# Optimization experiments

Measured on AMD Instinct MI355X. Metric: run time of the kernel, lower is better.

The kernel has to match this reference:

```python
import jax, jax.numpy as jnp
import numpy as np

DIM = 1024
HEADS = 16
HEAD_DIM = DIM // HEADS
B, N = 8, 1024


def setup_inputs() -> dict:
    key = jax.random.key(0)
    ks = jax.random.split(key, 10)
    s = lambda fan_in: 1.0 / np.sqrt(fan_in)
    return {
        "x": jax.random.normal(ks[0], (B, N, DIM), jnp.float32),
        "pose_angles": jax.random.normal(ks[1], (B, 3), jnp.float32),
        # weights stored (in, out) so y = x @ W + b (equivalent to torch Linear)
        "Wqkv": jax.random.normal(ks[2], (DIM, 3 * DIM), jnp.float32) * s(DIM),
        "bqkv": jnp.zeros((3 * DIM,), jnp.float32),
        "W1": jax.random.normal(ks[3], (3, 64), jnp.float32) * s(3),
        "b1": jnp.zeros((64,), jnp.float32),
        "W2": jax.random.normal(ks[4], (64, 3 * DIM), jnp.float32) * s(64),
        "b2": jnp.zeros((3 * DIM,), jnp.float32),
        "Wproj": jax.random.normal(ks[5], (DIM, DIM), jnp.float32) * s(DIM),
        "bproj": jnp.zeros((DIM,), jnp.float32),
    }


def reference(x, pose_angles, Wqkv, bqkv, W1, b1, W2, b2, Wproj, bproj):
    Bq, Nq, C = x.shape
    H, D = HEADS, HEAD_DIM
    # qkv projection -> [B,N,3,H,D] -> [3,B,H,N,D]
    qkv = (x @ Wqkv + bqkv).reshape(Bq, Nq, 3, H, D).transpose(2, 0, 3, 1, 4)
    q, k, v = qkv[0], qkv[1], qkv[2]
    # pose MLP: 3 -> 64 -> 3*dim, chunked into per-head biases [B,H,1,D]
    pose_emb = jax.nn.relu(pose_angles @ W1 + b1) @ W2 + b2
    pose_q, pose_k, pose_v = jnp.split(pose_emb, 3, axis=1)
    pose_q = pose_q.reshape(Bq, H, 1, D)
    pose_k = pose_k.reshape(Bq, H, 1, D)
    pose_v = pose_v.reshape(Bq, H, 1, D)
    q = q + pose_q
    k = k + pose_k
    v = v + pose_v
    scale = 1.0 / jnp.sqrt(jnp.asarray(D, x.dtype))
    attn = jax.nn.softmax(jnp.einsum("bhnd,bhmd->bhnm", q, k) * scale, axis=-1)
    # dropout is identity in eval mode
    out = jnp.einsum("bhnm,bhmd->bhnd", attn, v)
    out = out.transpose(0, 2, 1, 3).reshape(Bq, Nq, C)
    return out @ Wproj + bproj
```

## Files before the change

### kernel.cpp

```cpp
#include <hip/hip_runtime.h>
#include <stdint.h>

typedef unsigned short u16;
typedef short bf16x8 __attribute__((ext_vector_type(8)));
typedef short bf16x4 __attribute__((ext_vector_type(4)));
typedef float f32x4 __attribute__((ext_vector_type(4)));
typedef u16 u16x4 __attribute__((ext_vector_type(4)));

__device__ __forceinline__ u16 f2bf(float f) {
  union { float f; unsigned int u; } v; v.f = f;
  unsigned int r = v.u + 0x7fffu + ((v.u >> 16) & 1u);
  return (u16)(r >> 16);
}

__device__ __forceinline__ void async16(const void* g, void* l) {
  __builtin_amdgcn_global_load_lds(
      (const __attribute__((address_space(1))) unsigned int*)g,
      (__attribute__((address_space(3))) unsigned int*)l, 16, 0, 0);
}

__device__ __forceinline__ f32x4 mfma16x16(bf16x4 a, bf16x4 b, f32x4 c) {
#if __has_builtin(__builtin_amdgcn_mfma_f32_16x16x16bf16_1k)
  return __builtin_amdgcn_mfma_f32_16x16x16bf16_1k(a, b, c, 0, 0, 0);
#else
  asm volatile("v_mfma_f32_16x16x16_bf16 %0, %1, %2, %0\n\ts_nop 7\n\ts_nop 7"
               : "+v"(c) : "v"(a), "v"(b));
  return c;
#endif
}

__global__ void __launch_bounds__(256) front_kernel(
    const float4* __restrict__ x4, u16x4* __restrict__ xh4,
    const float* __restrict__ ang, const float* __restrict__ W1,
    const float* __restrict__ b1, const float* __restrict__ W2,
    const float* __restrict__ b2, float* __restrict__ pose,
    const float* __restrict__ Wqkv, u16* __restrict__ wqkvt,
    const float* __restrict__ Wproj, u16* __restrict__ wprojt) {
  __shared__ float sh[64 * 65];
  const int fb = blockIdx.x, t = threadIdx.x;
  if (fb < 96) {
    float (*hid)[64] = (float (*)[64])sh;
    for (int idx = t; idx < 512; idx += 256) {
      int b = idx >> 6, j = idx & 63;
      float a = b1[j];
#pragma unroll
      for (int i = 0; i < 3; ++i) a += ang[b * 3 + i] * W1[i * 64 + j];
      hid[b][j] = fmaxf(a, 0.f);
    }
    __syncthreads();
    int idx = fb * 256 + t;
    int b = idx / 3072, c = idx - b * 3072;
    float a = b2[c];
#pragma unroll
    for (int j = 0; j < 64; ++j) a += hid[b][j] * W2[j * 3072 + c];
    pose[idx] = a;
  } else if (fb < 1120) {
    const int n4 = 8 * 1024 * 1024 / 4;
    int i = (fb - 96) * 256 + t;
    const int stride = 1024 * 256;
    for (; i < n4; i += stride) {
      float4 v = x4[i];
      u16x4 o;
      o[0] = f2bf(v.x); o[1] = f2bf(v.y); o[2] = f2bf(v.z); o[3] = f2bf(v.w);
      xh4[i] = o;
    }
  } else {
    const float* W; u16* Wt; int Kdim, Ncol, bx, by;
    if (fb < 1888) { W = Wqkv; Wt = wqkvt; Kdim = 1024; Ncol = 3072;
                     int b = fb - 1120; bx = b % 48; by = b / 48; }
    else           { W = Wproj; Wt = wprojt; Kdim = 1024; Ncol = 1024;
                     int b = fb - 1888; bx = b % 16; by = b / 16; }
    float (*tile)[65] = (float (*)[65])sh;
    const int tx = t & 63, ty = t >> 6;
    const int c0 = bx * 64, k0 = by * 64;
#pragma unroll
    for (int rr = 0; rr < 16; ++rr) {
      int row = rr * 4 + ty;
      tile[row][tx] = W[(size_t)(k0 + row) * Ncol + c0 + tx];
    }
    __syncthreads();
#pragma unroll
    for (int rr = 0; rr < 16; ++rr) {
      int row = rr * 4 + ty;
      Wt[(size_t)(c0 + row) * Kdim + k0 + tx] = f2bf(tile[tx][row]);
    }
  }
}

template <int EPI>
__global__ void __launch_bounds__(512) gemm8_kernel(
    const u16* __restrict__ A, const u16* __restrict__ Bt,
    const float* __restrict__ bias, const float* __restrict__ pose,
    u16* __restrict__ qout, u16* __restrict__ kout, u16* __restrict__ vtout,
    float* __restrict__ cout, int Kdim, int Ncols, int nTilesX) {
  constexpr int BOFF = 256 * 64;
  __shared__ u16 lds[2][(256 + 128) * 64];
  const int t = threadIdx.x, l = t & 63, w = t >> 6;
  const int g = l >> 4, r16 = l & 15;
  const int wr = w >> 1, wc = w & 1;
  const int xk = r16 & 7;
  const int blk = blockIdx.x;
  const int xcd = blk & 7, c = blk >> 3;
  const int m0 = (xcd * 4 + (c & 3)) * 256;
  const int n0 = (c >> 2) * 128;
  (void)nTilesX;
  const u16* Ab = A + (size_t)m0 * Kdim;
  const u16* Bb = Bt + (size_t)n0 * Kdim;

  auto stage = [&](int buf, int kt, int st) {
#pragma unroll
    for (int it = 0; it < 2; ++it) {
      int idx = it * 512 + t, row = idx >> 3;
      int seg = (idx & 7) ^ (row & 7);
      if (st < 2)
        async16(Ab + (size_t)(st * 128 + row) * Kdim + kt + seg * 8,
                &lds[buf][st * 128 * 64 + idx * 8]);
      else
        async16(Bb + (size_t)row * Kdim + kt + seg * 8, &lds[buf][BOFF + idx * 8]);
    }
  };

  f32x4 acc[4][4] = {};
  const int nT = Kdim >> 6;
#pragma unroll
  for (int st = 0; st < 3; ++st) stage(0, 0, st);

  for (int tt = 0; tt < nT; ++tt) {
    const int cur = tt & 1, nxt = cur ^ 1;
    const bool pf = (tt + 1 < nT);
    const int ktn = (tt + 1) << 6;
    if (pf) {
      stage(nxt, ktn, 0);
      __builtin_amdgcn_sched_barrier(0);
      asm volatile("s_waitcnt vmcnt(2)" ::: "memory");
    } else {
      asm volatile("s_waitcnt vmcnt(0)" ::: "memory");
    }
    __builtin_amdgcn_s_barrier();
    __builtin_amdgcn_sched_barrier(0);
    bf16x8 bfr[4][2], af[2][2];
#pragma unroll
    for (int nj = 0; nj < 4; ++nj)
#pragma unroll
      for (int ks = 0; ks < 2; ++ks)
        bfr[nj][ks] = *(const bf16x8*)&lds[cur][BOFF + (wc * 64 + nj * 16 + r16) * 64 +
                                               ((ks * 4 + g) ^ xk) * 8];
#pragma unroll
    for (int mi = 0; mi < 2; ++mi)
#pragma unroll
      for (int ks = 0; ks < 2; ++ks)
        af[mi][ks] = *(const bf16x8*)&lds[cur][(wr * 64 + mi * 16 + r16) * 64 +
                                              ((ks * 4 + g) ^ xk) * 8];
    __builtin_amdgcn_s_setprio(1);
#pragma unroll
    for (int ks = 0; ks < 2; ++ks)
#pragma unroll
      for (int mi = 0; mi < 2; ++mi)
#pragma unroll
        for (int nj = 0; nj < 4; ++nj)
          acc[mi][nj] = __builtin_amdgcn_mfma_f32_16x16x32_bf16(af[mi][ks], bfr[nj][ks],
                                                                acc[mi][nj], 0, 0, 0);
    __builtin_amdgcn_s_setprio(0);
    if (pf) { stage(nxt, ktn, 1); stage(nxt, ktn, 2); }
    bf16x8 af2[2][2];
#pragma unroll
    for (int mi = 0; mi < 2; ++mi)
#pragma unroll
      for (int ks = 0; ks < 2; ++ks)
        af2[mi][ks] = *(const bf16x8*)&lds[cur][(wr * 64 + (mi + 2) * 16 + r16) * 64 +
                                               ((ks * 4 + g) ^ xk) * 8];
    __builtin_amdgcn_s_setprio(1);
#pragma unroll
    for (int ks = 0; ks < 2; ++ks)
#pragma unroll
      for (int mi = 0; mi < 2; ++mi)
#pragma unroll
        for (int nj = 0; nj < 4; ++nj)
          acc[mi + 2][nj] = __builtin_amdgcn_mfma_f32_16x16x32_bf16(af2[mi][ks], bfr[nj][ks],
                                                                    acc[mi + 2][nj], 0, 0, 0);
    __builtin_amdgcn_s_setprio(0);
    __builtin_amdgcn_s_barrier();
  }

#pragma unroll
  for (int mi = 0; mi < 4; ++mi)
#pragma unroll
    for (int nj = 0; nj < 4; ++nj)
#pragma unroll
      for (int r = 0; r < 4; ++r) {
        int row = m0 + wr * 64 + mi * 16 + g * 4 + r;
        int col = n0 + wc * 64 + nj * 16 + r16;
        float v = acc[mi][nj][r] + bias[col];
        if (EPI == 0) {
          int b = row >> 10, n = row & 1023;
          v += pose[b * 3072 + col];
          u16 hv = f2bf(v);
          int three = col >> 10, hh = (col >> 6) & 15, d = col & 63;
          size_t bhh = (size_t)(b * 16 + hh);
          if (three == 0)      qout[(bhh * 1024 + n) * 64 + d] = hv;
          else if (three == 1) kout[(bhh * 1024 + n) * 64 + d] = hv;
          else                 vtout[(bhh * 64 + d) * 1024 + n] = hv;
        } else {
          cout[(size_t)row * Ncols + col] = v;
        }
      }
}

__global__ void __launch_bounds__(256) attn_kernel(
    const u16* __restrict__ Qb, const u16* __restrict__ Kb,
    const u16* __restrict__ Vtb, u16* __restrict__ aout) {
  __shared__ u16 ldsK[2][64][72];
  __shared__ u16 ldsV[2][64][72];
  const int t = threadIdx.x, l = t & 63, w = t >> 6;
  const int g = l >> 4, r16 = l & 15;
  const int blk = blockIdx.x;
  const int bh = blk & 127, qt = blk >> 7;
  const int b = bh >> 4, h = bh & 15;
  const int q0 = qt * 64 + w * 16;
  const u16* Qp = Qb + ((size_t)bh * 1024 + q0 + r16) * 64;
  bf16x8 qreg0 = *(const bf16x8*)(Qp + g * 8);
  bf16x8 qreg1 = *(const bf16x8*)(Qp + 32 + g * 8);
  const u16* Kbase = Kb + (size_t)bh * 1024 * 64;
  const u16* Vbase = Vtb + (size_t)bh * 64 * 1024;
  const float cexp = 0.18033688f;

  const int row0 = t >> 3, seg0 = t & 7;
  const int row1 = (256 + t) >> 3, seg1 = t & 7;
  bf16x8 kreg0, kreg1, vreg0, vreg1;
  auto gload = [&](int key0) {
    kreg0 = *(const bf16x8*)(Kbase + (size_t)(key0 + row0) * 64 + seg0 * 8);
    vreg0 = *(const bf16x8*)(Vbase + (size_t)row0 * 1024 + key0 + seg0 * 8);
    kreg1 = *(const bf16x8*)(Kbase + (size_t)(key0 + row1) * 64 + seg1 * 8);
    vreg1 = *(const bf16x8*)(Vbase + (size_t)row1 * 1024 + key0 + seg1 * 8);
  };
  auto lwrite = [&](int buf) {
    *(bf16x8*)&ldsK[buf][row0][seg0 * 8] = kreg0;
    *(bf16x8*)&ldsV[buf][row0][seg0 * 8] = vreg0;
    *(bf16x8*)&ldsK[buf][row1][seg1 * 8] = kreg1;
    *(bf16x8*)&ldsV[buf][row1][seg1 * 8] = vreg1;
  };

  float m = -3e38f, rs = 0.f;
  f32x4 o[4] = {};
  gload(0); lwrite(0);
  __syncthreads();
  int cur = 0;
  for (int kt = 0; kt < 16; ++kt) {
    const bool pf = (kt + 1 < 16);
    if (pf) gload((kt + 1) * 64);
    f32x4 s[4] = {};
#pragma unroll
    for (int f = 0; f < 4; ++f) {
      bf16x8 ak0 = *(const bf16x8*)&ldsK[cur][f * 16 + r16][g * 8];
      s[f] = __builtin_amdgcn_mfma_f32_16x16x32_bf16(ak0, qreg0, s[f], 0, 0, 0);
      bf16x8 ak1 = *(const bf16x8*)&ldsK[cur][f * 16 + r16][32 + g * 8];
      s[f] = __builtin_amdgcn_mfma_f32_16x16x32_bf16(ak1, qreg1, s[f], 0, 0, 0);
    }
    float m01, m23, mt = -3e38f;
#pragma unroll
    for (int f = 0; f < 4; ++f) {
      m01 = fmaxf(s[f][0], s[f][1]);
      m23 = fmaxf(s[f][2], s[f][3]);
      mt = fmaxf(mt, fmaxf(m01, m23));
    }
    mt = fmaxf(mt, __shfl_xor(mt, 16));
    mt = fmaxf(mt, __shfl_xor(mt, 32));
    if (!__all(mt - m <= 64.f)) {
      float mnew = fmaxf(m, mt);
      float alpha = exp2f((m - mnew) * cexp);
      float ar[4];
#pragma unroll
      for (int r = 0; r < 4; ++r) ar[r] = __shfl(alpha, (l & 48) | (g * 4 + r));
#pragma unroll
      for (int nf = 0; nf < 4; ++nf)
#pragma unroll
        for (int r = 0; r < 4; ++r) o[nf][r] *= ar[r];
      rs *= alpha;
      m = mnew;
    }
    float rt = 0.f;
    bf16x4 pa[4];
#pragma unroll
    for (int f = 0; f < 4; ++f) {
#pragma unroll
      for (int r = 0; r < 4; ++r) {
        float p = exp2f((s[f][r] - m) * cexp);
        rt += p;
        pa[f][r] = (short)f2bf(p);
      }
    }
    rt += __shfl_xor(rt, 16);
    rt += __shfl_xor(rt, 32);
    rs += rt;
#pragma unroll
    for (int s4 = 0; s4 < 4; ++s4)
#pragma unroll
      for (int nf = 0; nf < 4; ++nf) {
        bf16x4 bv = *(const bf16x4*)&ldsV[cur][nf * 16 + r16][s4 * 16 + g * 4];
        o[nf] = mfma16x16(pa[s4], bv, o[nf]);
      }
    if (pf) lwrite(cur ^ 1);
    __syncthreads();
    cur ^= 1;
  }
  float rr[4];
#pragma unroll
  for (int r = 0; r < 4; ++r) rr[r] = __shfl(1.0f / rs, (l & 48) | (g * 4 + r));
#pragma unroll
  for (int nf = 0; nf < 4; ++nf)
#pragma unroll
    for (int r = 0; r < 4; ++r) {
      int qq = qt * 64 + w * 16 + g * 4 + r;
      int d = nf * 16 + r16;
      aout[((size_t)b * 1024 + qq) * 1024 + h * 64 + d] = f2bf(o[nf][r] * rr[r]);
    }
}

extern "C" void kernel_launch(void* const* d_in, const int* in_sizes, int n_in,
                              void* d_out, int out_size, void* d_ws, size_t ws_size,
                              hipStream_t stream) {
  (void)in_sizes; (void)n_in; (void)out_size; (void)ws_size;
  const float* x     = (const float*)d_in[0];
  const float* ang   = (const float*)d_in[1];
  const float* Wqkv  = (const float*)d_in[2];
  const float* bqkv  = (const float*)d_in[3];
  const float* W1    = (const float*)d_in[4];
  const float* b1    = (const float*)d_in[5];
  const float* W2    = (const float*)d_in[6];
  const float* b2    = (const float*)d_in[7];
  const float* Wproj = (const float*)d_in[8];
  const float* bproj = (const float*)d_in[9];
  float* out = (float*)d_out;
  char* ws = (char*)d_ws;

  u16* xh     = (u16*)(ws);
  u16* wqkvt  = (u16*)(ws + (size_t)16 * 1024 * 1024);
  u16* wprojt = (u16*)(ws + (size_t)22 * 1024 * 1024);
  float* pose = (float*)(ws + (size_t)24 * 1024 * 1024);
  u16* Qb     = (u16*)(ws + (size_t)25 * 1024 * 1024);
  u16* Kb     = (u16*)(ws + (size_t)41 * 1024 * 1024);
  u16* Vtb    = (u16*)(ws + (size_t)57 * 1024 * 1024);

  front_kernel<<<2144, 256, 0, stream>>>((const float4*)x, (u16x4*)xh,
                                         ang, W1, b1, W2, b2, pose,
                                         Wqkv, wqkvt, Wproj, wprojt);
  gemm8_kernel<0><<<768, 512, 0, stream>>>(xh, wqkvt, bqkv, pose,
                                           Qb, Kb, Vtb, nullptr, 1024, 3072, 24);
  attn_kernel<<<2048, 256, 0, stream>>>(Qb, Kb, Vtb, xh);
  gemm8_kernel<1><<<256, 512, 0, stream>>>(xh, wprojt, bproj, nullptr,
                                           nullptr, nullptr, nullptr, out, 1024, 1024, 8);
}
```

Baseline: 198.3 us.

## Replace double-buffered 256x128 GEMM with single-buffered 128x128 tile kernel

Both GEMMs switch from a 512-thread kernel with a 256x128 tile, double-buffered async LDS staging and priority hints to a simpler 256-thread kernel with a 128x128 tile and a single LDS buffer. Each K step loads, then syncs, then computes. The smaller tile doubles the block count and cuts LDS use per block, which could raise occupancy and help the smaller projection GEMM fill the GPU. In exchange it drops the load/compute overlap and reuses each loaded tile less, so the kernel will rely on having several blocks resident per CU to hide memory latency.

Result: faster. 194.1 us, median of 2 (-2.1%).

```diff
diff --git a/kernel.cpp b/kernel.cpp
--- a/kernel.cpp
+++ b/kernel.cpp
@@ -88,109 +88,66 @@
 }
 
 template <int EPI>
-__global__ void __launch_bounds__(512) gemm8_kernel(
+__global__ void __launch_bounds__(256) gemm97_kernel(
     const u16* __restrict__ A, const u16* __restrict__ Bt,
     const float* __restrict__ bias, const float* __restrict__ pose,
     u16* __restrict__ qout, u16* __restrict__ kout, u16* __restrict__ vtout,
-    float* __restrict__ cout, int Kdim, int Ncols, int nTilesX) {
-  constexpr int BOFF = 256 * 64;
-  __shared__ u16 lds[2][(256 + 128) * 64];
+    float* __restrict__ cout, int Kdim, int Ncols) {
+  __shared__ u16 ldsA[128 * 64];
+  __shared__ u16 ldsB[128 * 64];
   const int t = threadIdx.x, l = t & 63, w = t >> 6;
   const int g = l >> 4, r16 = l & 15;
   const int wr = w >> 1, wc = w & 1;
   const int xk = r16 & 7;
   const int blk = blockIdx.x;
   const int xcd = blk & 7, c = blk >> 3;
-  const int m0 = (xcd * 4 + (c & 3)) * 256;
-  const int n0 = (c >> 2) * 128;
-  (void)nTilesX;
+  const int m0 = (xcd * 8 + (c & 7)) * 128;
+  const int n0 = (c >> 3) * 128;
   const u16* Ab = A + (size_t)m0 * Kdim;
   const u16* Bb = Bt + (size_t)n0 * Kdim;
 
-  auto stage = [&](int buf, int kt, int st) {
-#pragma unroll
-    for (int it = 0; it < 2; ++it) {
-      int idx = it * 512 + t, row = idx >> 3;
+  f32x4 acc[4][4] = {};
+  for (int kt = 0; kt < Kdim; kt += 64) {
+#pragma unroll
+    for (int ii = 0; ii < 4; ++ii) {
+      int idx = ii * 256 + t, row = idx >> 3;
       int seg = (idx & 7) ^ (row & 7);
-      if (st < 2)
-        async16(Ab + (size_t)(st * 128 + row) * Kdim + kt + seg * 8,
-                &lds[buf][st * 128 * 64 + idx * 8]);
-      else
-        async16(Bb + (size_t)row * Kdim + kt + seg * 8, &lds[buf][BOFF + idx * 8]);
-    }
-  };
-
-  f32x4 acc[4][4] = {};
-  const int nT = Kdim >> 6;
-#pragma unroll
-  for (int st = 0; st < 3; ++st) stage(0, 0, st);
-
-  for (int tt = 0; tt < nT; ++tt) {
-    const int cur = tt & 1, nxt = cur ^ 1;
-    const bool pf = (tt + 1 < nT);
-    const int ktn = (tt + 1) << 6;
-    if (pf) {
-      stage(nxt, ktn, 0);
-      __builtin_amdgcn_sched_barrier(0);
-      asm volatile("s_waitcnt vmcnt(2)" ::: "memory");
-    } else {
-      asm volatile("s_waitcnt vmcnt(0)" ::: "memory");
-    }
-    __builtin_amdgcn_s_barrier();
-    __builtin_amdgcn_sched_barrier(0);
-    bf16x8 bfr[4][2], af[2][2];
-#pragma unroll
-    for (int nj = 0; nj < 4; ++nj)
-#pragma unroll
-      for (int ks = 0; ks < 2; ++ks)
-        bfr[nj][ks] = *(const bf16x8*)&lds[cur][BOFF + (wc * 64 + nj * 16 + r16) * 64 +
-                                               ((ks * 4 + g) ^ xk) * 8];
-#pragma unroll
-    for (int mi = 0; mi < 2; ++mi)
-#pragma unroll
-      for (int ks = 0; ks < 2; ++ks)
-        af[mi][ks] = *(const bf16x8*)&lds[cur][(wr * 64 + mi * 16 + r16) * 64 +
-                                              ((ks * 4 + g) ^ xk) * 8];
-    __builtin_amdgcn_s_setprio(1);
-#pragma unroll
-    for (int ks = 0; ks < 2; ++ks)
-#pragma unroll
-      for (int mi = 0; mi < 2; ++mi)
-#pragma unroll
-        for (int nj = 0; nj < 4; ++nj)
-          acc[mi][nj] = __builtin_amdgcn_mfma_f32_16x16x32_bf16(af[mi][ks], bfr[nj][ks],
-                                                                acc[mi][nj], 0, 0, 0);
-    __builtin_amdgcn_s_setprio(0);
-    if (pf) { stage(nxt, ktn, 1); stage(nxt, ktn, 2); }
-    bf16x8 af2[2][2];
-#pragma unroll
-    for (int mi = 0; mi < 2; ++mi)
-#pragma unroll
-      for (int ks = 0; ks < 2; ++ks)
-        af2[mi][ks] = *(const bf16x8*)&lds[cur][(wr * 64 + (mi + 2) * 16 + r16) * 64 +
-                                               ((ks * 4 + g) ^ xk) * 8];
-    __builtin_amdgcn_s_setprio(1);
-#pragma unroll
-    for (int ks = 0; ks < 2; ++ks)
-#pragma unroll
-      for (int mi = 0; mi < 2; ++mi)
-#pragma unroll
-        for (int nj = 0; nj < 4; ++nj)
-          acc[mi + 2][nj] = __builtin_amdgcn_mfma_f32_16x16x32_bf16(af2[mi][ks], bfr[nj][ks],
-                                                                    acc[mi + 2][nj], 0, 0, 0);
-    __builtin_amdgcn_s_setprio(0);
-    __builtin_amdgcn_s_barrier();
+      async16(Ab + (size_t)row * Kdim + kt + seg * 8, &ldsA[idx * 8]);
+    }
+#pragma unroll
+    for (int ii = 0; ii < 4; ++ii) {
+      int idx = ii * 256 + t, row = idx >> 3;
+      int seg = (idx & 7) ^ (row & 7);
+      async16(Bb + (size_t)row * Kdim + kt + seg * 8, &ldsB[idx * 8]);
+    }
+    __syncthreads();
+#pragma unroll
+    for (int ks = 0; ks < 2; ++ks) {
+      bf16x8 a[4], bb[4];
+#pragma unroll
+      for (int i = 0; i < 4; ++i)
+        a[i] = *(const bf16x8*)&ldsA[(wr * 64 + i * 16 + r16) * 64 + ((ks * 4 + g) ^ xk) * 8];
+#pragma unroll
+      for (int j = 0; j < 4; ++j)
+        bb[j] = *(const bf16x8*)&ldsB[(wc * 64 + j * 16 + r16) * 64 + ((ks * 4 + g) ^ xk) * 8];
+#pragma unroll
+      for (int i = 0; i < 4; ++i)
+#pragma unroll
+        for (int j = 0; j < 4; ++j)
+          acc[i][j] = __builtin_amdgcn_mfma_f32_16x16x32_bf16(a[i], bb[j], acc[i][j], 0, 0, 0);
+    }
+    __syncthreads();
   }
 
 #pragma unroll
-  for (int mi = 0; mi < 4; ++mi)
-#pragma unroll
-    for (int nj = 0; nj < 4; ++nj)
+  for (int i = 0; i < 4; ++i)
+#pragma unroll
+    for (int j = 0; j < 4; ++j)
 #pragma unroll
       for (int r = 0; r < 4; ++r) {
-        int row = m0 + wr * 64 + mi * 16 + g * 4 + r;
-        int col = n0 + wc * 64 + nj * 16 + r16;
-        float v = acc[mi][nj][r] + bias[col];
+        int row = m0 + wr * 64 + i * 16 + g * 4 + r;
+        int col = n0 + wc * 64 + j * 16 + r16;
+        float v = acc[i][j][r] + bias[col];
         if (EPI == 0) {
           int b = row >> 10, n = row & 1023;
           v += pose[b * 3072 + col];
@@ -344,9 +301,9 @@
   front_kernel<<<2144, 256, 0, stream>>>((const float4*)x, (u16x4*)xh,
                                          ang, W1, b1, W2, b2, pose,
                                          Wqkv, wqkvt, Wproj, wprojt);
-  gemm8_kernel<0><<<768, 512, 0, stream>>>(xh, wqkvt, bqkv, pose,
-                                           Qb, Kb, Vtb, nullptr, 1024, 3072, 24);
+  gemm97_kernel<0><<<1536, 256, 0, stream>>>(xh, wqkvt, bqkv, pose,
+                                             Qb, Kb, Vtb, nullptr, 1024, 3072);
   attn_kernel<<<2048, 256, 0, stream>>>(Qb, Kb, Vtb, xh);
-  gemm8_kernel<1><<<256, 512, 0, stream>>>(xh, wprojt, bproj, nullptr,
-                                           nullptr, nullptr, nullptr, out, 1024, 1024, 8);
-}
+  gemm97_kernel<1><<<512, 256, 0, stream>>>(xh, wprojt, bproj, nullptr,
+                                            nullptr, nullptr, nullptr, out, 1024, 1024);
+}
```

## Replace double-buffered pipelined GEMM with single-buffered LDS staging

Applied to the files above, without the earlier changes.

The GEMM kernel drops its two-stage LDS double buffer and the staggered prefetch of the next K tile. Each iteration now loads the whole A and B tile, synchronizes, computes all MFMAs, then synchronizes again. This halves LDS use per block, which may let more blocks fit per CU so that other blocks hide the memory latency. The cost is that load/compute overlap inside a block is lost, and there is more barrier stalling.

New measurement: 215.6 us. +8.7%, slower.

```diff
diff --git a/kernel.cpp b/kernel.cpp
--- a/kernel.cpp
+++ b/kernel.cpp
@@ -88,13 +88,13 @@
 }
 
 template <int EPI>
-__global__ void __launch_bounds__(512) gemm8_kernel(
+__global__ void __launch_bounds__(512) gemm_sb_kernel(
     const u16* __restrict__ A, const u16* __restrict__ Bt,
     const float* __restrict__ bias, const float* __restrict__ pose,
     u16* __restrict__ qout, u16* __restrict__ kout, u16* __restrict__ vtout,
-    float* __restrict__ cout, int Kdim, int Ncols, int nTilesX) {
+    float* __restrict__ cout, int Kdim, int Ncols) {
   constexpr int BOFF = 256 * 64;
-  __shared__ u16 lds[2][(256 + 128) * 64];
+  __shared__ u16 lds[(256 + 128) * 64];
   const int t = threadIdx.x, l = t & 63, w = t >> 6;
   const int g = l >> 4, r16 = l & 15;
   const int wr = w >> 1, wc = w & 1;
@@ -103,83 +103,56 @@
   const int xcd = blk & 7, c = blk >> 3;
   const int m0 = (xcd * 4 + (c & 3)) * 256;
   const int n0 = (c >> 2) * 128;
-  (void)nTilesX;
   const u16* Ab = A + (size_t)m0 * Kdim;
   const u16* Bb = Bt + (size_t)n0 * Kdim;
 
-  auto stage = [&](int buf, int kt, int st) {
-#pragma unroll
-    for (int it = 0; it < 2; ++it) {
-      int idx = it * 512 + t, row = idx >> 3;
-      int seg = (idx & 7) ^ (row & 7);
-      if (st < 2)
-        async16(Ab + (size_t)(st * 128 + row) * Kdim + kt + seg * 8,
-                &lds[buf][st * 128 * 64 + idx * 8]);
-      else
-        async16(Bb + (size_t)row * Kdim + kt + seg * 8, &lds[buf][BOFF + idx * 8]);
-    }
-  };
-
   f32x4 acc[4][4] = {};
   const int nT = Kdim >> 6;
-#pragma unroll
-  for (int st = 0; st < 3; ++st) stage(0, 0, st);
-
   for (int tt = 0; tt < nT; ++tt) {
-    const int cur = tt & 1, nxt = cur ^ 1;
-    const bool pf = (tt + 1 < nT);
-    const int ktn = (tt + 1) << 6;
-    if (pf) {
-      stage(nxt, ktn, 0);
-      __builtin_amdgcn_sched_barrier(0);
-      asm volatile("s_waitcnt vmcnt(2)" ::: "memory");
-    } else {
-      asm volatile("s_waitcnt vmcnt(0)" ::: "memory");
-    }
-    __builtin_amdgcn_s_barrier();
-    __builtin_amdgcn_sched_barrier(0);
-    bf16x8 bfr[4][2], af[2][2];
+    const int kt = tt << 6;
+#pragma unroll
+    for (int st = 0; st < 3; ++st)
+#pragma unroll
+      for (int it = 0; it < 2; ++it) {
+        int idx = it * 512 + t, row = idx >> 3;
+        int seg = (idx & 7) ^ (row & 7);
+        if (st < 2)
+          async16(Ab + (size_t)(st * 128 + row) * Kdim + kt + seg * 8,
+                  &lds[st * 128 * 64 + idx * 8]);
+        else
+          async16(Bb + (size_t)row * Kdim + kt + seg * 8, &lds[BOFF + idx * 8]);
+      }
+    __syncthreads();
+    bf16x8 bfr[4][2], af[2][2], af2[2][2];
 #pragma unroll
     for (int nj = 0; nj < 4; ++nj)
 #pragma unroll
       for (int ks = 0; ks < 2; ++ks)
-        bfr[nj][ks] = *(const bf16x8*)&lds[cur][BOFF + (wc * 64 + nj * 16 + r16) * 64 +
-                                               ((ks * 4 + g) ^ xk) * 8];
+        bfr[nj][ks] = *(const bf16x8*)&lds[BOFF + (wc * 64 + nj * 16 + r16) * 64 +
+                                          ((ks * 4 + g) ^ xk) * 8];
 #pragma unroll
     for (int mi = 0; mi < 2; ++mi)
 #pragma unroll
-      for (int ks = 0; ks < 2; ++ks)
-        af[mi][ks] = *(const bf16x8*)&lds[cur][(wr * 64 + mi * 16 + r16) * 64 +
-                                              ((ks * 4 + g) ^ xk) * 8];
+      for (int ks = 0; ks < 2; ++ks) {
+        af[mi][ks] = *(const bf16x8*)&lds[(wr * 64 + mi * 16 + r16) * 64 +
+                                         ((ks * 4 + g) ^ xk) * 8];
+        af2[mi][ks] = *(const bf16x8*)&lds[(wr * 64 + (mi + 2) * 16 + r16) * 64 +
+                                          ((ks * 4 + g) ^ xk) * 8];
+      }
     __builtin_amdgcn_s_setprio(1);
 #pragma unroll
     for (int ks = 0; ks < 2; ++ks)
 #pragma unroll
       for (int mi = 0; mi < 2; ++mi)
 #pragma unroll
-        for (int nj = 0; nj < 4; ++nj)
+        for (int nj = 0; nj < 4; ++nj) {
           acc[mi][nj] = __builtin_amdgcn_mfma_f32_16x16x32_bf16(af[mi][ks], bfr[nj][ks],
                                                                 acc[mi][nj], 0, 0, 0);
-    __builtin_amdgcn_s_setprio(0);
-    if (pf) { stage(nxt, ktn, 1); stage(nxt, ktn, 2); }
-    bf16x8 af2[2][2];
-#pragma unroll
-    for (int mi = 0; mi < 2; ++mi)
-#pragma unroll
-      for (int ks = 0; ks < 2; ++ks)
-        af2[mi][ks] = *(const bf16x8*)&lds[cur][(wr * 64 + (mi + 2) * 16 + r16) * 64 +
-                                               ((ks * 4 + g) ^ xk) * 8];
-    __builtin_amdgcn_s_setprio(1);
-#pragma unroll
-    for (int ks = 0; ks < 2; ++ks)
-#pragma unroll
-      for (int mi = 0; mi < 2; ++mi)
-#pragma unroll
-        for (int nj = 0; nj < 4; ++nj)
           acc[mi + 2][nj] = __builtin_amdgcn_mfma_f32_16x16x32_bf16(af2[mi][ks], bfr[nj][ks],
                                                                     acc[mi + 2][nj], 0, 0, 0);
+        }
     __builtin_amdgcn_s_setprio(0);
-    __builtin_amdgcn_s_barrier();
+    __syncthreads();
   }
 
 #pragma unroll
@@ -344,9 +317,9 @@
   front_kernel<<<2144, 256, 0, stream>>>((const float4*)x, (u16x4*)xh,
                                          ang, W1, b1, W2, b2, pose,
                                          Wqkv, wqkvt, Wproj, wprojt);
-  gemm8_kernel<0><<<768, 512, 0, stream>>>(xh, wqkvt, bqkv, pose,
-                                           Qb, Kb, Vtb, nullptr, 1024, 3072, 24);
+  gemm_sb_kernel<0><<<768, 512, 0, stream>>>(xh, wqkvt, bqkv, pose,
+                                             Qb, Kb, Vtb, nullptr, 1024, 3072);
   attn_kernel<<<2048, 256, 0, stream>>>(Qb, Kb, Vtb, xh);
-  gemm8_kernel<1><<<256, 512, 0, stream>>>(xh, wprojt, bproj, nullptr,
-                                           nullptr, nullptr, nullptr, out, 1024, 1024, 8);
-}
+  gemm_sb_kernel<1><<<256, 512, 0, stream>>>(xh, wprojt, bproj, nullptr,
+                                             nullptr, nullptr, nullptr, out, 1024, 1024);
+}
```

## Use dedicated 128x128-tile GEMM for output projection to raise block count

Applied to the files above, without the earlier changes.

The output projection previously reused the 256x128-tile, 512-thread double-buffered GEMM, launching only 256 blocks for an 8192x1024 output. It now gets a separate simpler kernel with 128x128 tiles and 256 threads, giving 512 blocks so more CUs are covered. The new kernel is single-buffered and syncs twice per k-step, so it gives up load/compute overlap in exchange for the extra parallelism. The QKV GEMM template is specialised to its one epilogue.

Result: no change. 201.9 us (+1.8%).

```diff
diff --git a/kernel.cpp b/kernel.cpp
--- a/kernel.cpp
+++ b/kernel.cpp
@@ -87,12 +87,11 @@
   }
 }
 
-template <int EPI>
 __global__ void __launch_bounds__(512) gemm8_kernel(
     const u16* __restrict__ A, const u16* __restrict__ Bt,
     const float* __restrict__ bias, const float* __restrict__ pose,
     u16* __restrict__ qout, u16* __restrict__ kout, u16* __restrict__ vtout,
-    float* __restrict__ cout, int Kdim, int Ncols, int nTilesX) {
+    int Kdim) {
   constexpr int BOFF = 256 * 64;
   __shared__ u16 lds[2][(256 + 128) * 64];
   const int t = threadIdx.x, l = t & 63, w = t >> 6;
@@ -103,7 +102,6 @@
   const int xcd = blk & 7, c = blk >> 3;
   const int m0 = (xcd * 4 + (c & 3)) * 256;
   const int n0 = (c >> 2) * 128;
-  (void)nTilesX;
   const u16* Ab = A + (size_t)m0 * Kdim;
   const u16* Bb = Bt + (size_t)n0 * Kdim;
 
@@ -191,18 +189,76 @@
         int row = m0 + wr * 64 + mi * 16 + g * 4 + r;
         int col = n0 + wc * 64 + nj * 16 + r16;
         float v = acc[mi][nj][r] + bias[col];
-        if (EPI == 0) {
-          int b = row >> 10, n = row & 1023;
-          v += pose[b * 3072 + col];
-          u16 hv = f2bf(v);
-          int three = col >> 10, hh = (col >> 6) & 15, d = col & 63;
-          size_t bhh = (size_t)(b * 16 + hh);
-          if (three == 0)      qout[(bhh * 1024 + n) * 64 + d] = hv;
-          else if (three == 1) kout[(bhh * 1024 + n) * 64 + d] = hv;
-          else                 vtout[(bhh * 64 + d) * 1024 + n] = hv;
-        } else {
-          cout[(size_t)row * Ncols + col] = v;
-        }
+        int b = row >> 10, n = row & 1023;
+        v += pose[b * 3072 + col];
+        u16 hv = f2bf(v);
+        int three = col >> 10, hh = (col >> 6) & 15, d = col & 63;
+        size_t bhh = (size_t)(b * 16 + hh);
+        if (three == 0)      qout[(bhh * 1024 + n) * 64 + d] = hv;
+        else if (three == 1) kout[(bhh * 1024 + n) * 64 + d] = hv;
+        else                 vtout[(bhh * 64 + d) * 1024 + n] = hv;
+      }
+}
+
+__global__ void __launch_bounds__(256) gemm97_kernel(
+    const u16* __restrict__ A, const u16* __restrict__ Bt,
+    const float* __restrict__ bias, float* __restrict__ cout,
+    int Kdim, int Ncols) {
+  __shared__ u16 ldsA[128 * 64];
+  __shared__ u16 ldsB[128 * 64];
+  const int t = threadIdx.x, l = t & 63, w = t >> 6;
+  const int g = l >> 4, r16 = l & 15;
+  const int wr = w >> 1, wc = w & 1;
+  const int xk = r16 & 7;
+  const int blk = blockIdx.x;
+  const int xcd = blk & 7, c = blk >> 3;
+  const int m0 = (xcd * 8 + (c & 7)) * 128;
+  const int n0 = (c >> 3) * 128;
+  const u16* Ab = A + (size_t)m0 * Kdim;
+  const u16* Bb = Bt + (size_t)n0 * Kdim;
+
+  f32x4 acc[4][4] = {};
+  for (int kt = 0; kt < Kdim; kt += 64) {
+#pragma unroll
+    for (int ii = 0; ii < 4; ++ii) {
+      int idx = ii * 256 + t, row = idx >> 3;
+      int seg = (idx & 7) ^ (row & 7);
+      async16(Ab + (size_t)row * Kdim + kt + seg * 8, &ldsA[idx * 8]);
+    }
+#pragma unroll
+    for (int ii = 0; ii < 4; ++ii) {
+      int idx = ii * 256 + t, row = idx >> 3;
+      int seg = (idx & 7) ^ (row & 7);
+      async16(Bb + (size_t)row * Kdim + kt + seg * 8, &ldsB[idx * 8]);
+    }
+    __syncthreads();
+#pragma unroll
+    for (int ks = 0; ks < 2; ++ks) {
+      bf16x8 a[4], bb[4];
+#pragma unroll
+      for (int i = 0; i < 4; ++i)
+        a[i] = *(const bf16x8*)&ldsA[(wr * 64 + i * 16 + r16) * 64 + ((ks * 4 + g) ^ xk) * 8];
+#pragma unroll
+      for (int j = 0; j < 4; ++j)
+        bb[j] = *(const bf16x8*)&ldsB[(wc * 64 + j * 16 + r16) * 64 + ((ks * 4 + g) ^ xk) * 8];
+#pragma unroll
+      for (int i = 0; i < 4; ++i)
+#pragma unroll
+        for (int j = 0; j < 4; ++j)
+          acc[i][j] = __builtin_amdgcn_mfma_f32_16x16x32_bf16(a[i], bb[j], acc[i][j], 0, 0, 0);
+    }
+    __syncthreads();
+  }
+
+#pragma unroll
+  for (int i = 0; i < 4; ++i)
+#pragma unroll
+    for (int j = 0; j < 4; ++j)
+#pragma unroll
+      for (int r = 0; r < 4; ++r) {
+        int row = m0 + wr * 64 + i * 16 + g * 4 + r;
+        int col = n0 + wc * 64 + j * 16 + r16;
+        cout[(size_t)row * Ncols + col] = acc[i][j][r] + bias[col];
       }
 }
 
@@ -344,9 +400,8 @@
   front_kernel<<<2144, 256, 0, stream>>>((const float4*)x, (u16x4*)xh,
                                          ang, W1, b1, W2, b2, pose,
                                          Wqkv, wqkvt, Wproj, wprojt);
-  gemm8_kernel<0><<<768, 512, 0, stream>>>(xh, wqkvt, bqkv, pose,
-                                           Qb, Kb, Vtb, nullptr, 1024, 3072, 24);
+  gemm8_kernel<<<768, 512, 0, stream>>>(xh, wqkvt, bqkv, pose,
+                                        Qb, Kb, Vtb, 1024);
   attn_kernel<<<2048, 256, 0, stream>>>(Qb, Kb, Vtb, xh);
-  gemm8_kernel<1><<<256, 512, 0, stream>>>(xh, wprojt, bproj, nullptr,
-                                           nullptr, nullptr, nullptr, out, 1024, 1024, 8);
-}
+  gemm97_kernel<<<512, 256, 0, stream>>>(xh, wprojt, bproj, out, 1024, 1024);
+}
```
